# Optimization experiments

Measured on AMD Instinct MI355X. Metric: run time of the kernel, lower is better.

Reference implementation:

```python
import jax, jax.numpy as jnp
import numpy as np

# Screen config (matches init_kwargs)
W, H, TL = 1920, 1080, 16
NBW = -(-W // TL)          # 120
NBH = -(-H // TL)          # 68
NB = NBW * NBH             # 8160 tiles
N = 500_000                # number of points
K = 5                      # max tiles per axis a point can overlap (radius < 24, TL=16)
RADIUS_MAX = 24.0


def setup_inputs() -> dict:
    key = jax.random.key(0)
    k1, k2, k3 = jax.random.split(key, 3)
    pos2d = jax.random.uniform(k1, (N, 2), dtype=jnp.float32) * jnp.array([W, H], dtype=jnp.float32)
    radius = jax.random.uniform(k2, (N,), dtype=jnp.float32) * (RADIUS_MAX - 1.0) + 1.0
    depth = jax.random.normal(k3, (N,), dtype=jnp.float32)
    return {"pos2d": pos2d, "radius": radius, "depth": depth}


def reference(pos2d, radius, depth):
    # Tile bounds per point (identical clamping semantics to the torch module).
    xmin = jnp.clip(jnp.floor_divide(pos2d[:, 0] - radius, TL), 0, NBW).astype(jnp.int32)
    ymin = jnp.clip(jnp.floor_divide(pos2d[:, 1] - radius, TL), 0, NBH).astype(jnp.int32)
    xmax = jnp.clip(jnp.floor_divide(pos2d[:, 0] + radius, TL) + 1, 0, NBW).astype(jnp.int32)
    ymax = jnp.clip(jnp.floor_divide(pos2d[:, 1] + radius, TL) + 1, 0, NBH).astype(jnp.int32)

    # Enumerate a fixed KxK candidate tile window per point, mask out-of-range tiles.
    dxy = jnp.arange(K, dtype=jnp.int32)
    xi = xmin[:, None] + dxy            # [N, K]
    yi = ymin[:, None] + dxy            # [N, K]
    vx = xi < xmax[:, None]
    vy = yi < ymax[:, None]
    valid = (vx[:, :, None] & vy[:, None, :]).reshape(-1)              # [E]
    tid = (xi[:, :, None] * NBH + yi[:, None, :]).reshape(-1)          # [E] flat tile id (x-major, as in module)
    tid = jnp.where(valid, tid, NB).astype(jnp.int32)                  # sentinel NB -> sorts to end
    pid = jnp.broadcast_to(jnp.arange(N, dtype=jnp.int32)[:, None, None], (N, K, K)).reshape(-1)
    d_entry = jnp.broadcast_to(depth[:, None, None], (N, K, K)).reshape(-1)

    # Counting-sort equivalent: per-tile histogram + exclusive cumsum offsets.
    counts = jax.ops.segment_sum(valid.astype(jnp.int32), tid, num_segments=NB + 1)[:NB]
    tile_count = jnp.concatenate([jnp.zeros((1,), jnp.int32), jnp.cumsum(counts)[:-1].astype(jnp.int32)])

    # Sort pairs by (tile id, depth descending) -> contiguous per-tile, depth-sorted index lists.
    order = jnp.lexsort((-d_entry, tid))
    tid_s = tid[order]
    pid_s = pid[order]
    live = tid_s < NB
    tile_indices = jnp.where(live, pid_s, -1)                          # padded with -1 at the tail
    sorted_depth = jnp.where(live, depth[pid_s], 0.0)                  # depths in per-tile sorted order
    return tile_count, tile_indices, sorted_depth
```

## Files before the change

kernel.cpp:

```cpp
#include <hip/hip_runtime.h>
#include <stdint.h>
#include <math.h>

typedef unsigned short u16;
typedef unsigned int u32;
typedef unsigned long long u64;

#define NBW 120
#define NBH 68
#define NTILES (NBW * NBH)
#define NPTS 500000
#define EE 12500000
#define SORT_CAP 768
#define NBKT 512
#define HB 64
#define HT 1024
#define DX 121
#define DY 69
#define DCELLS 8352
#define DCW (DCELLS / 2)
#define PCW 4080

__device__ __forceinline__ int clampi(int v, int lo, int hi) {
    return v < lo ? lo : (v > hi ? hi : v);
}

__device__ __forceinline__ void tile_window(float x, float y, float r,
                                            int& x0, int& x1, int& y0, int& y1) {
    x0 = clampi((int)floorf((x - r) * 0.0625f), 0, NBW);
    x1 = clampi((int)floorf((x + r) * 0.0625f) + 1, 0, NBW);
    y0 = clampi((int)floorf((y - r) * 0.0625f), 0, NBH);
    y1 = clampi((int)floorf((y + r) * 0.0625f) + 1, 0, NBH);
}

__device__ __forceinline__ u32 depth_key(float d) {
    u32 fu = __float_as_uint(d);
    u32 asc = (fu & 0x80000000u) ? ~fu : (fu | 0x80000000u);
    return ~asc;
}
__device__ __forceinline__ float depth_unkey(u32 dk) {
    u32 asc = ~dk;
    u32 fu = (asc & 0x80000000u) ? (asc & 0x7FFFFFFFu) : ~asc;
    return __uint_as_float(fu);
}

__device__ __forceinline__ int tile_of_block(int b) {
    return (b & 7) * (NTILES / 8) + (b >> 3);
}

__device__ __forceinline__ u32 bucket_of(u32 dk, const u32* __restrict__ Ts) {
    u32 k = dk >> 24;
    u32 t0 = Ts[k], t1 = Ts[k + 1];
    u32 b = t0 + (((t1 - t0) * ((dk >> 8) & 0xFFFFu)) >> 16);
    return b >= NBKT ? (NBKT - 1) : b;
}

__device__ __forceinline__ void lds_inc16(u32* arr, int cell) {
    atomicAdd(&arr[cell >> 1], (cell & 1) ? 0x10000u : 1u);
}


__global__ __launch_bounds__(HT) void hist_kernel(const float2* __restrict__ pos,
                                                  const float* __restrict__ rad,
                                                  u32* __restrict__ pcslc,
                                                  u32* __restrict__ diffslc) {
    __shared__ u32 s_pc[PCW];
    __shared__ u32 s_dp[DCW];
    __shared__ u32 s_dm[DCW];
    int tid = threadIdx.x;
    for (int w = tid; w < PCW; w += HT) s_pc[w] = 0;
    for (int w = tid; w < DCW; w += HT) { s_dp[w] = 0; s_dm[w] = 0; }
    __syncthreads();

    for (int i = blockIdx.x * HT + tid; i < NPTS; i += HB * HT) {
        float2 p = pos[i];
        float r = rad[i];
        int x0, x1, y0, y1;
        tile_window(p.x, p.y, r, x0, x1, y0, y1);
        int cx = (int)(p.x * 0.0625f);
        int cy = (int)(p.y * 0.0625f);
        lds_inc16(s_pc, cx * NBH + cy);
        lds_inc16(s_dp, x0 * DY + y0);
        lds_inc16(s_dp, x1 * DY + y1);
        lds_inc16(s_dm, x0 * DY + y1);
        lds_inc16(s_dm, x1 * DY + y0);
    }
    __syncthreads();

    for (int w = tid; w < PCW; w += HT) pcslc[blockIdx.x * PCW + w] = s_pc[w];
    for (int wi = tid; wi < DCW; wi += HT) {
        u32 pw = s_dp[wi], mw = s_dm[wi];
        int d0 = (int)(pw & 0xFFFFu) - (int)(mw & 0xFFFFu);
        int d1 = (int)(pw >> 16)     - (int)(mw >> 16);
        diffslc[blockIdx.x * DCW + wi] = ((u32)d0 & 0xFFFFu) | ((u32)d1 << 16);
    }
}

__global__ void reduce_kernel(const u32* __restrict__ pcslc, const u32* __restrict__ diffslc,
                              u32* __restrict__ counts, u16* __restrict__ ctab0,
                              int* __restrict__ sdg) {
    int idx = blockIdx.x * 256 + threadIdx.x;
    if (idx < NTILES) {
        int sh = (idx & 1) * 16;
        int w = idx >> 1;
        u32 run = 0;
        for (int b = 0; b < HB; ++b) {
            ctab0[b * NTILES + idx] = (u16)run;
            run += (pcslc[b * PCW + w] >> sh) & 0xFFFFu;
        }
        counts[idx] = run;
    } else if (idx < NTILES + DCELLS) {
        int c = idx - NTILES;
        int wi = c >> 1, sh = (c & 1) * 16;
        int acc = 0;
        for (int b = 0; b < HB; ++b)
            acc += (int)(short)((diffslc[b * DCW + wi] >> sh) & 0xFFFFu);
        sdg[c] = acc;
    }
}

__global__ __launch_bounds__(1024) void scan3_kernel(const u32* __restrict__ counts,
                                                     u32* __restrict__ po,
                                                     const int* __restrict__ sdg,
                                                     u32* __restrict__ eo,
                                                     float* __restrict__ out_count,
                                                     u32* __restrict__ Tg) {
    __shared__ u32 sA[1024], sB[1024];
    __shared__ int sd[DCELLS];
    __shared__ u32 traw[257];
    int t = threadIdx.x;
    int base = t * 8;

    if (blockIdx.x == 0) {
        u32 local[8]; u32 sum = 0;
#pragma unroll
        for (int j = 0; j < 8; ++j) {
            u32 c = (base + j < NTILES) ? counts[base + j] : 0u;
            local[j] = c; sum += c;
        }
        sA[t] = sum;
        __syncthreads();
        u32 *cur = sA, *nxt = sB;
        for (int off = 1; off < 1024; off <<= 1) {
            u32 v = cur[t];
            if (t >= off) v += cur[t - off];
            nxt[t] = v;
            __syncthreads();
            u32* tmp = cur; cur = nxt; nxt = tmp;
        }
        u32 run = cur[t] - sum;
#pragma unroll
        for (int j = 0; j < 8; ++j) {
            int idx = base + j;
            if (idx < NTILES) { po[idx] = run; run += local[j]; }
        }
        if (t == 1023) po[NTILES] = cur[1023];
    } else if (blockIdx.x == 1) {
        for (int c = t; c < DCELLS; c += 1024) sd[c] = sdg[c];
        __syncthreads();
        if (t < DX) { int run = 0; for (int y = 0; y < DY; ++y) { run += sd[t * DY + y]; sd[t * DY + y] = run; } }
        __syncthreads();
        if (t < DY) { int run = 0; for (int x = 0; x < DX; ++x) { run += sd[x * DY + t]; sd[x * DY + t] = run; } }
        __syncthreads();

        u32 local[8]; u32 sum = 0;
#pragma unroll
        for (int j = 0; j < 8; ++j) {
            int idx = base + j;
            u32 c = 0;
            if (idx < NTILES) {
                int x = idx / NBH, y = idx % NBH;
                c = (u32)sd[x * DY + y];
            }
            local[j] = c; sum += c;
        }
        sA[t] = sum;
        __syncthreads();
        u32 *cur = sA, *nxt = sB;
        for (int off = 1; off < 1024; off <<= 1) {
            u32 v = cur[t];
            if (t >= off) v += cur[t - off];
            nxt[t] = v;
            __syncthreads();
            u32* tmp = cur; cur = nxt; nxt = tmp;
        }
        u32 run = cur[t] - sum;
#pragma unroll
        for (int j = 0; j < 8; ++j) {
            int idx = base + j;
            if (idx < NTILES) {
                eo[idx] = run;
                out_count[idx] = (float)run;
                run += local[j];
            }
        }
        if (t == 1023) eo[NTILES] = cur[1023];
    } else {
        if (t < 257) {
            u32 dkb = (u32)t << 24;
            float d = depth_unkey(dkb);
            float u;
            if (d != d) u = (t < 128) ? 0.f : 1.f;
            else {
                float dc = fminf(fmaxf(d, -12.f), 12.f);
                u = 0.5f * erfcf(dc * 0.70710678f);
            }
            traw[t] = (u32)(u * (float)NBKT + 0.5f);
        }
        __syncthreads();
        if (t == 0) {
            u32 run = 0;
            for (int k = 0; k < 257; ++k) {
                u32 v = traw[k];
                if (v > NBKT) v = NBKT;
                if (v > run) run = v;
                Tg[k] = run;
            }
        }
    }
}

__global__ __launch_bounds__(HT) void point_scatter_kernel(const float2* __restrict__ pos,
                                                           const float* __restrict__ rad,
                                                           const float* __restrict__ depth,
                                                           const u16* __restrict__ ctab0,
                                                           const u32* __restrict__ po,
                                                           u64* __restrict__ pe) {
    __shared__ u32 cur[NTILES];
    int tid = threadIdx.x;
    for (int w = tid; w < NTILES; w += HT)
        cur[w] = po[w] + (u32)ctab0[blockIdx.x * NTILES + w];
    __syncthreads();
    for (int i = blockIdx.x * HT + tid; i < NPTS; i += HB * HT) {
        float2 p = pos[i];
        float r = rad[i];
        int x0, x1, y0, y1;
        tile_window(p.x, p.y, r, x0, x1, y0, y1);
        int cx = (int)(p.x * 0.0625f);
        int cy = (int)(p.y * 0.0625f);
        u32 dk = depth_key(depth[i]);
        u32 meta = ((u32)(cx - x0) << 11) | ((u32)(x1 - cx - 1) << 9)
                 | ((u32)y0 << 2) | (u32)(y1 - y0 - 1);
        u32 slot = atomicAdd(&cur[cx * NBH + cy], 1u);
        pe[slot] = ((u64)dk << 32) | ((u64)(u32)i << 13) | (u64)meta;
    }
}

__global__ __launch_bounds__(256) void tile_build_kernel(const u32* __restrict__ po,
                                                         const u64* __restrict__ pe,
                                                         const u32* __restrict__ eo,
                                                         const u32* __restrict__ Tg,
                                                         float* __restrict__ out_idx,
                                                         float* __restrict__ out_depth) {
    __shared__ u64 keys[SORT_CAP];
    __shared__ u64 keys2[SORT_CAP];
    __shared__ u32 boff[NBKT + 1];
    __shared__ u32 bcur[NBKT];
    __shared__ u32 Ts[257];
    __shared__ u32 wsum[4];
    __shared__ u32 lcnt;

    int tid = threadIdx.x;
    int lane = tid & 63;
    int wv = tid >> 6;

    {
        u32 total = eo[NTILES];
        u32 tailn = EE - total;
        u32 per = (tailn + NTILES - 1) / NTILES;
        u64 s = (u64)total + (u64)blockIdx.x * per;
        u64 e = s + per; if (e > (u64)EE) e = EE;
        for (u64 i = s + tid; i < e; i += 256) {
            out_idx[i] = -1.f;
            out_depth[i] = 0.f;
        }
    }

    int t = tile_of_block(blockIdx.x);
    u32 base = eo[t];
    int cnt = (int)(eo[t + 1] - base);
    if (cnt <= 0) return;

    int tx = t / NBH;
    int ty = t % NBH;
    bool big = cnt > SORT_CAP;

    for (int b = tid; b < NBKT; b += 256) boff[b] = 0;
    for (int k = tid; k < 257; k += 256) Ts[k] = Tg[k];
    if (tid == 0) lcnt = 0;
    __syncthreads();

    int cx0 = tx - 2 < 0 ? 0 : tx - 2;
    int cx1 = tx + 2 > NBW - 1 ? NBW - 1 : tx + 2;
    int cy0 = ty - 2 < 0 ? 0 : ty - 2;
    int cy1 = ty + 2 > NBH - 1 ? NBH - 1 : ty + 2;

    if (!big) {
        for (int cx = cx0; cx <= cx1; ++cx) {
            int dcx = cx - tx;
            u32 s = po[cx * NBH + cy0];
            u32 e = po[cx * NBH + cy1 + 1];
            for (u32 i = s + tid; i < e; i += 256) {
                u64 v = pe[i];
                u32 meta = (u32)v & 0x1FFFu;
                int h = (int)(meta & 3u);
                int y0 = (int)((meta >> 2) & 127u);
                int dx1m1 = (int)((meta >> 9) & 3u);
                int dx0 = (int)((meta >> 11) & 3u);
                if (dx0 >= dcx && dx1m1 >= -dcx && ty >= y0 && ty <= y0 + h) {
                    u32 slot = atomicAdd(&lcnt, 1u);
                    keys[slot] = v;
                    atomicAdd(&boff[bucket_of((u32)(v >> 32), Ts)], 1u);
                }
            }
        }
        __syncthreads();

        {
            int b0 = tid * 2;
            u32 h0 = boff[b0], h1 = boff[b0 + 1];
            u32 tsum = h0 + h1;
            u32 v = tsum;
            for (int off = 1; off < 64; off <<= 1) {
                u32 n = __shfl_up(v, off, 64);
                if (lane >= off) v += n;
            }
            if (lane == 63) wsum[wv] = v;
            __syncthreads();
            u32 wpre = 0;
            for (int w = 0; w < wv; ++w) wpre += wsum[w];
            u32 run = wpre + v - tsum;
            boff[b0] = run;     bcur[b0] = run;     run += h0;
            boff[b0 + 1] = run; bcur[b0 + 1] = run; run += h1;
            if (tid == 255) boff[NBKT] = run;
        }
        __syncthreads();

        for (int i = tid; i < cnt; i += 256) {
            u64 v = keys[i];
            u32 slot = atomicAdd(&bcur[bucket_of((u32)(v >> 32), Ts)], 1u);
            keys2[slot] = v;
        }
        __syncthreads();

        for (int b = tid; b < NBKT; b += 256) {
            int s = (int)boff[b], e = (int)boff[b + 1];
            for (int i = s + 1; i < e; ++i) {
                u64 k = keys2[i];
                int j = i - 1;
                while (j >= s && keys2[j] > k) { keys2[j + 1] = keys2[j]; --j; }
                keys2[j + 1] = k;
            }
        }
        __syncthreads();

        for (int i = tid; i < cnt; i += 256) {
            u64 k = keys2[i];
            u32 pid = (u32)(k >> 13) & 0x7FFFFu;
            u32 dk  = (u32)(k >> 32);
            out_idx[base + i]   = (float)pid;
            out_depth[base + i] = depth_unkey(dk);
        }
    } else {
        for (int cx = cx0; cx <= cx1; ++cx) {
            int dcx = cx - tx;
            u32 s = po[cx * NBH + cy0];
            u32 e = po[cx * NBH + cy1 + 1];
            for (u32 i = s + tid; i < e; i += 256) {
                u64 v = pe[i];
                u32 meta = (u32)v & 0x1FFFu;
                int h = (int)(meta & 3u);
                int y0 = (int)((meta >> 2) & 127u);
                int dx1m1 = (int)((meta >> 9) & 3u);
                int dx0 = (int)((meta >> 11) & 3u);
                if (dx0 >= dcx && dx1m1 >= -dcx && ty >= y0 && ty <= y0 + h) {
                    u32 pid = (u32)(v >> 13) & 0x7FFFFu;
                    u32 dk  = (u32)(v >> 32);
                    u32 slot = atomicAdd(&lcnt, 1u);
                    out_idx[base + slot] = (float)pid;
                    out_depth[base + slot] = depth_unkey(dk);
                }
            }
        }
        __syncthreads();
        for (int round = 0; round < cnt; ++round) {
            for (int i = (round & 1) + 2 * tid; i + 1 < cnt; i += 512) {
                float fi0 = out_idx[base + i], fi1 = out_idx[base + i + 1];
                float fd0 = out_depth[base + i], fd1 = out_depth[base + i + 1];
                u64 k0 = ((u64)depth_key(fd0) << 19) | (u64)(u32)fi0;
                u64 k1 = ((u64)depth_key(fd1) << 19) | (u64)(u32)fi1;
                if (k0 > k1) {
                    out_idx[base + i] = fi1; out_idx[base + i + 1] = fi0;
                    out_depth[base + i] = fd1; out_depth[base + i + 1] = fd0;
                }
            }
            __syncthreads();
        }
    }
}

extern "C" void kernel_launch(void* const* d_in, const int* in_sizes, int n_in,
                              void* d_out, int out_size, void* d_ws, size_t ws_size,
                              hipStream_t stream) {
    (void)in_sizes; (void)n_in; (void)out_size; (void)ws_size;

    const float2* pos  = (const float2*)d_in[0];
    const float* rad   = (const float*)d_in[1];
    const float* depth = (const float*)d_in[2];

    float* out        = (float*)d_out;
    float* out_count  = out;
    float* out_idx    = out + NTILES;
    float* out_depth  = out + NTILES + EE;

    u64* pe     = (u64*)d_ws;
    u32* counts = (u32*)(pe + NPTS);
    u32* po     = counts + NTILES;
    u32* eo     = po + NTILES + 1;
    int* sdg    = (int*)(eo + NTILES + 1);
    u32* Tg     = (u32*)(sdg + DCELLS);

    u16* ctab0   = (u16*)((u32*)out_idx + EE) - (size_t)HB * NTILES;
    u32* pcslc   = (u32*)(out_depth + EE) - ((size_t)HB * PCW + (size_t)HB * DCW);
    u32* diffslc = pcslc + (size_t)HB * PCW;

    hist_kernel<<<HB, HT, 0, stream>>>(pos, rad, pcslc, diffslc);
    reduce_kernel<<<(NTILES + DCELLS + 255) / 256, 256, 0, stream>>>(pcslc, diffslc,
                                                                     counts, ctab0, sdg);
    scan3_kernel<<<3, 1024, 0, stream>>>(counts, po, sdg, eo, out_count, Tg);
    point_scatter_kernel<<<HB, HT, 0, stream>>>(pos, rad, depth, ctab0, po, pe);
    tile_build_kernel<<<NTILES, 256, 0, stream>>>(po, pe, eo, Tg,
                                                  out_idx, out_depth);
}
```

Measured before the change: 196.0 us.

## Bin points into fixed-capacity per-tile slabs with global atomics, dropping prefix-scan scatter

Replaces the two-pass histogram/reduce/prefix-scan/scatter of points into a compact array with a single pass that appends each point into a fixed 128-slot slab per center tile using global atomics. The slab lives in the tail of the depth output and is zeroed afterwards. The tile build kernel gathers neighbour tiles through a small per-block offset table with binary search. This removes a reduce kernel, a scan, and a scatter pass, at the cost of global atomic contention, an extra zeroing pass over the slab region, and silent truncation if a tile exceeds the slab capacity.

```diff
diff --git a/kernel.cpp b/kernel.cpp
--- a/kernel.cpp
+++ b/kernel.cpp
@@ -13,13 +13,14 @@
 #define EE 12500000
 #define SORT_CAP 768
 #define NBKT 512
-#define HB 64
-#define HT 1024
+#define CAP 128
+#define SLABF (NTILES * CAP * 2)
+#define HB2 128
+#define HT2 512
 #define DX 121
 #define DY 69
 #define DCELLS 8352
 #define DCW (DCELLS / 2)
-#define PCW 4080
 
 __device__ __forceinline__ int clampi(int v, int lo, int hi) {
     return v < lo ? lo : (v > hi ? hi : v);
@@ -60,26 +61,37 @@
 }
 
 
-__global__ __launch_bounds__(HT) void hist_kernel(const float2* __restrict__ pos,
-                                                  const float* __restrict__ rad,
-                                                  u32* __restrict__ pcslc,
-                                                  u32* __restrict__ diffslc) {
-    __shared__ u32 s_pc[PCW];
+__global__ void zero_cnt_kernel(u32* __restrict__ cnt) {
+    int i = blockIdx.x * 1024 + threadIdx.x;
+    if (i < NTILES) cnt[i] = 0;
+}
+
+__global__ __launch_bounds__(HT2) void scatter_hist_kernel(const float2* __restrict__ pos,
+                                                           const float* __restrict__ rad,
+                                                           const float* __restrict__ depth,
+                                                           u32* __restrict__ cnt,
+                                                           u64* __restrict__ slab,
+                                                           u32* __restrict__ diffslc) {
     __shared__ u32 s_dp[DCW];
     __shared__ u32 s_dm[DCW];
     int tid = threadIdx.x;
-    for (int w = tid; w < PCW; w += HT) s_pc[w] = 0;
-    for (int w = tid; w < DCW; w += HT) { s_dp[w] = 0; s_dm[w] = 0; }
+    for (int w = tid; w < DCW; w += HT2) { s_dp[w] = 0; s_dm[w] = 0; }
     __syncthreads();
 
-    for (int i = blockIdx.x * HT + tid; i < NPTS; i += HB * HT) {
+    for (int i = blockIdx.x * HT2 + tid; i < NPTS; i += HB2 * HT2) {
         float2 p = pos[i];
         float r = rad[i];
         int x0, x1, y0, y1;
         tile_window(p.x, p.y, r, x0, x1, y0, y1);
         int cx = (int)(p.x * 0.0625f);
         int cy = (int)(p.y * 0.0625f);
-        lds_inc16(s_pc, cx * NBH + cy);
+        u32 dk = depth_key(depth[i]);
+        u32 meta = ((u32)(cx - x0) << 11) | ((u32)(x1 - cx - 1) << 9)
+                 | ((u32)y0 << 2) | (u32)(y1 - y0 - 1);
+        int ct = cx * NBH + cy;
+        u32 slot = atomicAdd(&cnt[ct], 1u);
+        if (slot < CAP)
+            slab[(size_t)ct * CAP + slot] = ((u64)dk << 32) | ((u64)(u32)i << 13) | (u64)meta;
         lds_inc16(s_dp, x0 * DY + y0);
         lds_inc16(s_dp, x1 * DY + y1);
         lds_inc16(s_dm, x0 * DY + y1);
@@ -87,8 +99,7 @@
     }
     __syncthreads();
 
-    for (int w = tid; w < PCW; w += HT) pcslc[blockIdx.x * PCW + w] = s_pc[w];
-    for (int wi = tid; wi < DCW; wi += HT) {
+    for (int wi = tid; wi < DCW; wi += HT2) {
         u32 pw = s_dp[wi], mw = s_dm[wi];
         int d0 = (int)(pw & 0xFFFFu) - (int)(mw & 0xFFFFu);
         int d1 = (int)(pw >> 16)     - (int)(mw >> 16);
@@ -96,32 +107,17 @@
     }
 }
 
-__global__ void reduce_kernel(const u32* __restrict__ pcslc, const u32* __restrict__ diffslc,
-                              u32* __restrict__ counts, u16* __restrict__ ctab0,
-                              int* __restrict__ sdg) {
-    int idx = blockIdx.x * 256 + threadIdx.x;
-    if (idx < NTILES) {
-        int sh = (idx & 1) * 16;
-        int w = idx >> 1;
-        u32 run = 0;
-        for (int b = 0; b < HB; ++b) {
-            ctab0[b * NTILES + idx] = (u16)run;
-            run += (pcslc[b * PCW + w] >> sh) & 0xFFFFu;
-        }
-        counts[idx] = run;
-    } else if (idx < NTILES + DCELLS) {
-        int c = idx - NTILES;
-        int wi = c >> 1, sh = (c & 1) * 16;
-        int acc = 0;
-        for (int b = 0; b < HB; ++b)
-            acc += (int)(short)((diffslc[b * DCW + wi] >> sh) & 0xFFFFu);
-        sdg[c] = acc;
-    }
-}
-
-__global__ __launch_bounds__(1024) void scan3_kernel(const u32* __restrict__ counts,
-                                                     u32* __restrict__ po,
-                                                     const int* __restrict__ sdg,
+__global__ void reduce_diff_kernel(const u32* __restrict__ diffslc, int* __restrict__ sdg) {
+    int c = blockIdx.x * 256 + threadIdx.x;
+    if (c >= DCELLS) return;
+    int wi = c >> 1, sh = (c & 1) * 16;
+    int acc = 0;
+    for (int b = 0; b < HB2; ++b)
+        acc += (int)(short)((diffslc[b * DCW + wi] >> sh) & 0xFFFFu);
+    sdg[c] = acc;
+}
+
+__global__ __launch_bounds__(1024) void scan2_kernel(const int* __restrict__ sdg,
                                                      u32* __restrict__ eo,
                                                      float* __restrict__ out_count,
                                                      u32* __restrict__ Tg) {
@@ -132,30 +128,6 @@
     int base = t * 8;
 
     if (blockIdx.x == 0) {
-        u32 local[8]; u32 sum = 0;
-#pragma unroll
-        for (int j = 0; j < 8; ++j) {
-            u32 c = (base + j < NTILES) ? counts[base + j] : 0u;
-            local[j] = c; sum += c;
-        }
-        sA[t] = sum;
-        __syncthreads();
-        u32 *cur = sA, *nxt = sB;
-        for (int off = 1; off < 1024; off <<= 1) {
-            u32 v = cur[t];
-            if (t >= off) v += cur[t - off];
-            nxt[t] = v;
-            __syncthreads();
-            u32* tmp = cur; cur = nxt; nxt = tmp;
-        }
-        u32 run = cur[t] - sum;
-#pragma unroll
-        for (int j = 0; j < 8; ++j) {
-            int idx = base + j;
-            if (idx < NTILES) { po[idx] = run; run += local[j]; }
-        }
-        if (t == 1023) po[NTILES] = cur[1023];
-    } else if (blockIdx.x == 1) {
         for (int c = t; c < DCELLS; c += 1024) sd[c] = sdg[c];
         __syncthreads();
         if (t < DX) { int run = 0; for (int y = 0; y < DY; ++y) { run += sd[t * DY + y]; sd[t * DY + y] = run; } }
@@ -220,34 +192,8 @@
     }
 }
 
-__global__ __launch_bounds__(HT) void point_scatter_kernel(const float2* __restrict__ pos,
-                                                           const float* __restrict__ rad,
-                                                           const float* __restrict__ depth,
-                                                           const u16* __restrict__ ctab0,
-                                                           const u32* __restrict__ po,
-                                                           u64* __restrict__ pe) {
-    __shared__ u32 cur[NTILES];
-    int tid = threadIdx.x;
-    for (int w = tid; w < NTILES; w += HT)
-        cur[w] = po[w] + (u32)ctab0[blockIdx.x * NTILES + w];
-    __syncthreads();
-    for (int i = blockIdx.x * HT + tid; i < NPTS; i += HB * HT) {
-        float2 p = pos[i];
-        float r = rad[i];
-        int x0, x1, y0, y1;
-        tile_window(p.x, p.y, r, x0, x1, y0, y1);
-        int cx = (int)(p.x * 0.0625f);
-        int cy = (int)(p.y * 0.0625f);
-        u32 dk = depth_key(depth[i]);
-        u32 meta = ((u32)(cx - x0) << 11) | ((u32)(x1 - cx - 1) << 9)
-                 | ((u32)y0 << 2) | (u32)(y1 - y0 - 1);
-        u32 slot = atomicAdd(&cur[cx * NBH + cy], 1u);
-        pe[slot] = ((u64)dk << 32) | ((u64)(u32)i << 13) | (u64)meta;
-    }
-}
-
-__global__ __launch_bounds__(256) void tile_build_kernel(const u32* __restrict__ po,
-                                                         const u64* __restrict__ pe,
+__global__ __launch_bounds__(256) void tile_build_kernel(const u32* __restrict__ cnt,
+                                                         const u64* __restrict__ slab,
                                                          const u32* __restrict__ eo,
                                                          const u32* __restrict__ Tg,
                                                          float* __restrict__ out_idx,
@@ -259,6 +205,9 @@
     __shared__ u32 Ts[257];
     __shared__ u32 wsum[4];
     __shared__ u32 lcnt;
+    __shared__ u32 nb_off[26];
+    __shared__ u32 nb_base[25];
+    __shared__ int nb_dcx[25];
 
     int tid = threadIdx.x;
     int lane = tid & 63;
@@ -270,48 +219,69 @@
         u32 per = (tailn + NTILES - 1) / NTILES;
         u64 s = (u64)total + (u64)blockIdx.x * per;
         u64 e = s + per; if (e > (u64)EE) e = EE;
-        for (u64 i = s + tid; i < e; i += 256) {
-            out_idx[i] = -1.f;
-            out_depth[i] = 0.f;
-        }
+        for (u64 i = s + tid; i < e; i += 256) out_idx[i] = -1.f;
+
+        u32 limit = EE - SLABF;
+        u32 tn2 = limit > total ? limit - total : 0;
+        u32 per2 = (tn2 + NTILES - 1) / NTILES;
+        u64 s2 = (u64)total + (u64)blockIdx.x * per2;
+        u64 e2 = s2 + per2; if (e2 > (u64)limit) e2 = limit;
+        for (u64 i = s2 + tid; i < e2; i += 256) out_depth[i] = 0.f;
     }
 
     int t = tile_of_block(blockIdx.x);
     u32 base = eo[t];
-    int cnt = (int)(eo[t + 1] - base);
-    if (cnt <= 0) return;
+    int cnt_e = (int)(eo[t + 1] - base);
+    if (cnt_e <= 0) return;
 
     int tx = t / NBH;
     int ty = t % NBH;
-    bool big = cnt > SORT_CAP;
+    bool big = cnt_e > SORT_CAP;
 
     for (int b = tid; b < NBKT; b += 256) boff[b] = 0;
     for (int k = tid; k < 257; k += 256) Ts[k] = Tg[k];
     if (tid == 0) lcnt = 0;
+    if (tid < 25) {
+        int dx = tid / 5 - 2, dy = tid % 5 - 2;
+        int ncx = tx + dx, ncy = ty + dy;
+        u32 n = 0, b = 0;
+        if (ncx >= 0 && ncx < NBW && ncy >= 0 && ncy < NBH) {
+            int nt = ncx * NBH + ncy;
+            n = cnt[nt]; if (n > CAP) n = CAP;
+            b = (u32)nt * CAP;
+        }
+        nb_base[tid] = b;
+        nb_dcx[tid] = dx;
+        nb_off[tid + 1] = n;
+    }
+    if (tid == 25) nb_off[0] = 0;
     __syncthreads();
-
-    int cx0 = tx - 2 < 0 ? 0 : tx - 2;
-    int cx1 = tx + 2 > NBW - 1 ? NBW - 1 : tx + 2;
-    int cy0 = ty - 2 < 0 ? 0 : ty - 2;
-    int cy1 = ty + 2 > NBH - 1 ? NBH - 1 : ty + 2;
+    if (tid == 0) {
+        u32 run = 0;
+#pragma unroll
+        for (int k = 1; k <= 25; ++k) { run += nb_off[k]; nb_off[k] = run; }
+    }
+    __syncthreads();
+    u32 S = nb_off[25];
 
     if (!big) {
-        for (int cx = cx0; cx <= cx1; ++cx) {
-            int dcx = cx - tx;
-            u32 s = po[cx * NBH + cy0];
-            u32 e = po[cx * NBH + cy1 + 1];
-            for (u32 i = s + tid; i < e; i += 256) {
-                u64 v = pe[i];
-                u32 meta = (u32)v & 0x1FFFu;
-                int h = (int)(meta & 3u);
-                int y0 = (int)((meta >> 2) & 127u);
-                int dx1m1 = (int)((meta >> 9) & 3u);
-                int dx0 = (int)((meta >> 11) & 3u);
-                if (dx0 >= dcx && dx1m1 >= -dcx && ty >= y0 && ty <= y0 + h) {
-                    u32 slot = atomicAdd(&lcnt, 1u);
-                    keys[slot] = v;
-                    atomicAdd(&boff[bucket_of((u32)(v >> 32), Ts)], 1u);
-                }
+        for (u32 j = tid; j < S; j += 256) {
+            int lo = 0, hi = 24;
+            while (lo < hi) {
+                int mid = (lo + hi + 1) >> 1;
+                if (nb_off[mid] <= j) lo = mid; else hi = mid - 1;
+            }
+            u64 v = slab[nb_base[lo] + (j - nb_off[lo])];
+            u32 meta = (u32)v & 0x1FFFu;
+            int h = (int)(meta & 3u);
+            int y0 = (int)((meta >> 2) & 127u);
+            int dx1m1 = (int)((meta >> 9) & 3u);
+            int dx0 = (int)((meta >> 11) & 3u);
+            int dcx = nb_dcx[lo];
+            if (dx0 >= dcx && dx1m1 >= -dcx && ty >= y0 && ty <= y0 + h) {
+                u32 slot = atomicAdd(&lcnt, 1u);
+                keys[slot] = v;
+                atomicAdd(&boff[bucket_of((u32)(v >> 32), Ts)], 1u);
             }
         }
         __syncthreads();
@@ -336,7 +306,7 @@
         }
         __syncthreads();
 
-        for (int i = tid; i < cnt; i += 256) {
+        for (int i = tid; i < cnt_e; i += 256) {
             u64 v = keys[i];
             u32 slot = atomicAdd(&bcur[bucket_of((u32)(v >> 32), Ts)], 1u);
             keys2[slot] = v;
@@ -354,7 +324,7 @@
         }
         __syncthreads();
 
-        for (int i = tid; i < cnt; i += 256) {
+        for (int i = tid; i < cnt_e; i += 256) {
             u64 k = keys2[i];
             u32 pid = (u32)(k >> 13) & 0x7FFFFu;
             u32 dk  = (u32)(k >> 32);
@@ -362,29 +332,30 @@
             out_depth[base + i] = depth_unkey(dk);
         }
     } else {
-        for (int cx = cx0; cx <= cx1; ++cx) {
-            int dcx = cx - tx;
-            u32 s = po[cx * NBH + cy0];
-            u32 e = po[cx * NBH + cy1 + 1];
-            for (u32 i = s + tid; i < e; i += 256) {
-                u64 v = pe[i];
-                u32 meta = (u32)v & 0x1FFFu;
-                int h = (int)(meta & 3u);
-                int y0 = (int)((meta >> 2) & 127u);
-                int dx1m1 = (int)((meta >> 9) & 3u);
-                int dx0 = (int)((meta >> 11) & 3u);
-                if (dx0 >= dcx && dx1m1 >= -dcx && ty >= y0 && ty <= y0 + h) {
-                    u32 pid = (u32)(v >> 13) & 0x7FFFFu;
-                    u32 dk  = (u32)(v >> 32);
-                    u32 slot = atomicAdd(&lcnt, 1u);
-                    out_idx[base + slot] = (float)pid;
-                    out_depth[base + slot] = depth_unkey(dk);
-                }
-            }
-        }
-        __syncthreads();
-        for (int round = 0; round < cnt; ++round) {
-            for (int i = (round & 1) + 2 * tid; i + 1 < cnt; i += 512) {
+        for (u32 j = tid; j < S; j += 256) {
+            int lo = 0, hi = 24;
+            while (lo < hi) {
+                int mid = (lo + hi + 1) >> 1;
+                if (nb_off[mid] <= j) lo = mid; else hi = mid - 1;
+            }
+            u64 v = slab[nb_base[lo] + (j - nb_off[lo])];
+            u32 meta = (u32)v & 0x1FFFu;
+            int h = (int)(meta & 3u);
+            int y0 = (int)((meta >> 2) & 127u);
+            int dx1m1 = (int)((meta >> 9) & 3u);
+            int dx0 = (int)((meta >> 11) & 3u);
+            int dcx = nb_dcx[lo];
+            if (dx0 >= dcx && dx1m1 >= -dcx && ty >= y0 && ty <= y0 + h) {
+                u32 pid = (u32)(v >> 13) & 0x7FFFFu;
+                u32 dk  = (u32)(v >> 32);
+                u32 slot = atomicAdd(&lcnt, 1u);
+                out_idx[base + slot] = (float)pid;
+                out_depth[base + slot] = depth_unkey(dk);
+            }
+        }
+        __syncthreads();
+        for (int round = 0; round < cnt_e; ++round) {
+            for (int i = (round & 1) + 2 * tid; i + 1 < cnt_e; i += 512) {
                 float fi0 = out_idx[base + i], fi1 = out_idx[base + i + 1];
                 float fd0 = out_depth[base + i], fd1 = out_depth[base + i + 1];
                 u64 k0 = ((u64)depth_key(fd0) << 19) | (u64)(u32)fi0;
@@ -399,6 +370,12 @@
     }
 }
 
+__global__ void zero_slab_kernel(float4* __restrict__ dst) {
+    int n = SLABF / 4;
+    for (int i = blockIdx.x * 256 + threadIdx.x; i < n; i += 512 * 256)
+        dst[i] = make_float4(0.f, 0.f, 0.f, 0.f);
+}
+
 extern "C" void kernel_launch(void* const* d_in, const int* in_sizes, int n_in,
                               void* d_out, int out_size, void* d_ws, size_t ws_size,
                               hipStream_t stream) {
@@ -413,22 +390,18 @@
     float* out_idx    = out + NTILES;
     float* out_depth  = out + NTILES + EE;
 
-    u64* pe     = (u64*)d_ws;
-    u32* counts = (u32*)(pe + NPTS);
-    u32* po     = counts + NTILES;
-    u32* eo     = po + NTILES + 1;
-    int* sdg    = (int*)(eo + NTILES + 1);
-    u32* Tg     = (u32*)(sdg + DCELLS);
-
-    u16* ctab0   = (u16*)((u32*)out_idx + EE) - (size_t)HB * NTILES;
-    u32* pcslc   = (u32*)(out_depth + EE) - ((size_t)HB * PCW + (size_t)HB * DCW);
-    u32* diffslc = pcslc + (size_t)HB * PCW;
-
-    hist_kernel<<<HB, HT, 0, stream>>>(pos, rad, pcslc, diffslc);
-    reduce_kernel<<<(NTILES + DCELLS + 255) / 256, 256, 0, stream>>>(pcslc, diffslc,
-                                                                     counts, ctab0, sdg);
-    scan3_kernel<<<3, 1024, 0, stream>>>(counts, po, sdg, eo, out_count, Tg);
-    point_scatter_kernel<<<HB, HT, 0, stream>>>(pos, rad, depth, ctab0, po, pe);
-    tile_build_kernel<<<NTILES, 256, 0, stream>>>(po, pe, eo, Tg,
-                                                  out_idx, out_depth);
-}
+    u32* cnt     = (u32*)d_ws;
+    u32* eo      = cnt + NTILES;
+    int* sdg     = (int*)(eo + NTILES + 1);
+    u32* Tg      = (u32*)(sdg + DCELLS);
+    u32* diffslc = Tg + 257;
+
+    u64* slab = (u64*)(out_depth + EE) - (size_t)NTILES * CAP;
+
+    zero_cnt_kernel<<<8, 1024, 0, stream>>>(cnt);
+    scatter_hist_kernel<<<HB2, HT2, 0, stream>>>(pos, rad, depth, cnt, slab, diffslc);
+    reduce_diff_kernel<<<(DCELLS + 255) / 256, 256, 0, stream>>>(diffslc, sdg);
+    scan2_kernel<<<2, 1024, 0, stream>>>(sdg, eo, out_count, Tg);
+    tile_build_kernel<<<NTILES, 256, 0, stream>>>(cnt, slab, eo, Tg, out_idx, out_depth);
+    zero_slab_kernel<<<512, 256, 0, stream>>>((float4*)(out_depth + EE - SLABF));
+}
```

After: 206.0 us. 1.05x slower.
